# Optimization experiments

Hardware: AMD Instinct MI355X
Metric: run time of the kernel (lower is better)

The kernel has to match this reference:

```python
import jax, jax.numpy as jnp
import numpy as np
from jax import lax

B, T, C = 1, 2048, 2048
HS = 64
H = C // HS          # 32 heads
FFN = 7168
NS = 4               # packed sequences in the batch-1 stream
EPS_LN = 1e-5
EPS_GN = 1e-5 * 8 ** 2   # GroupNorm eps = 1e-5 * head_size_divisor**2


def setup_inputs() -> dict:
    key = jax.random.key(0)
    ks = iter(jax.random.split(key, 48))
    def rn(shape, s=1.0):
        return jax.random.normal(next(ks), shape, jnp.float32) * s
    sc = C ** -0.5
    return dict(
        x=rn((B, T, C)),
        start_pos=jnp.array([0, 512, 1024, 1536], dtype=jnp.int32),
        att_state=rn((NS, C)),
        wkv_state=rn((NS, H, HS, HS), 0.1),
        ffn_state=rn((NS, C)),
        ln1_g=jnp.ones((C,), jnp.float32), ln1_b=jnp.zeros((C,), jnp.float32),
        ln2_g=jnp.ones((C,), jnp.float32), ln2_b=jnp.zeros((C,), jnp.float32),
        tm_maa_x=rn((C,), 0.1), tm_maa_w=rn((C,), 0.1), tm_maa_k=rn((C,), 0.1),
        tm_maa_v=rn((C,), 0.1), tm_maa_r=rn((C,), 0.1), tm_maa_g=rn((C,), 0.1),
        tm_w1=rn((C, 160), 0.02), tm_w2=rn((5, 32, C), 0.02),
        td=rn((C,), 0.3) - 0.5, td_w1=rn((C, 64), 0.02), td_w2=rn((64, C), 0.02),
        u=rn((H, HS), 0.1),
        Wr=rn((C, C), sc), Wk=rn((C, C), sc), Wv=rn((C, C), sc),
        Wg=rn((C, C), sc), Wo=rn((C, C), sc),
        lnx_g=jnp.ones((C,), jnp.float32), lnx_b=jnp.zeros((C,), jnp.float32),
        cm_maa_k=rn((C,), 0.1), cm_maa_r=rn((C,), 0.1),
        Wck=rn((C, FFN), sc), Wcv=rn((FFN, C), FFN ** -0.5), Wcr=rn((C, C), sc),
    )


def _ln(x, g, b, eps):
    m = x.mean(-1, keepdims=True)
    v = ((x - m) ** 2).mean(-1, keepdims=True)
    return (x - m) * lax.rsqrt(v + eps) * g + b


def _shift(x, start_pos, state):
    # ZeroPad2d((0,0,1,-1)) token shift, then restore per-sequence carry state
    sh = jnp.concatenate([jnp.zeros_like(x[:, :1]), x[:, :-1]], axis=1)
    return sh.at[0, start_pos, :].set(state)


def reference(x, start_pos, att_state, wkv_state, ffn_state,
              ln1_g, ln1_b, ln2_g, ln2_b,
              tm_maa_x, tm_maa_w, tm_maa_k, tm_maa_v, tm_maa_r, tm_maa_g,
              tm_w1, tm_w2, td, td_w1, td_w2, u,
              Wr, Wk, Wv, Wg, Wo, lnx_g, lnx_b,
              cm_maa_k, cm_maa_r, Wck, Wcv, Wcr):
    is_start = jnp.zeros((T,), bool).at[start_pos].set(True)
    seq_id = jnp.clip(jnp.cumsum(is_start.astype(jnp.int32)) - 1, 0, NS - 1)

    # ---------------- Tmix (RWKV6 time mix) ----------------
    xa = _ln(x, ln1_g, ln1_b, EPS_LN)
    sh = _shift(xa, start_pos, att_state)
    xx = sh - xa
    xxx = jnp.tanh((xa + xx * tm_maa_x) @ tm_w1)                    # [B,T,160]
    mix = jnp.einsum('btse,sec->sbtc', xxx.reshape(B, T, 5, 32), tm_w2)
    mw, mk, mv, mr, mg = mix
    xw = xa + xx * (tm_maa_w + mw)
    xk = xa + xx * (tm_maa_k + mk)
    xv = xa + xx * (tm_maa_v + mv)
    xr = xa + xx * (tm_maa_r + mr)
    xg = xa + xx * (tm_maa_g + mg)
    r = (xr @ Wr).reshape(T, H, HS)
    k = (xk @ Wk).reshape(T, H, HS)
    v = (xv @ Wv).reshape(T, H, HS)
    g = jax.nn.silu(xg @ Wg)                                        # [B,T,C]
    w = td + jnp.tanh(xw @ td_w1) @ td_w2                           # [B,T,C]
    dec = jnp.exp(-jnp.exp(w)).reshape(T, H, HS)

    # continuous WKV recurrence: per-sequence state restore at starts
    def step(S, inp):
        rt, kt, vt, dt, st, sid = inp
        S = jnp.where(st, wkv_state[sid], S)                        # [H,HS,HS]
        y = jnp.einsum('hi,hij->hj', rt, S) \
            + (rt * u * kt).sum(-1, keepdims=True) * vt             # bonus term
        S = dt[:, :, None] * S + kt[:, :, None] * vt[:, None, :]
        return S, y

    _, y = lax.scan(step, jnp.zeros((H, HS, HS), jnp.float32),
                    (r, k, v, dec, is_start, seq_id))
    y = y.reshape(B, T, H, HS)
    # GroupNorm (n_head groups) fused per token/head
    mu = y.mean(-1, keepdims=True)
    var = ((y - mu) ** 2).mean(-1, keepdims=True)
    y = ((y - mu) * lax.rsqrt(var + EPS_GN)).reshape(B, T, C) * lnx_g + lnx_b
    x = x + (y * g) @ Wo

    # ---------------- CMix (channel mix) ----------------
    xf = _ln(x, ln2_g, ln2_b, EPS_LN)
    sh = _shift(xf, start_pos, ffn_state)
    xx = sh - xf
    xk = xf + xx * cm_maa_k
    xr = xf + xx * cm_maa_r
    kv = jnp.square(jax.nn.relu(xk @ Wck)) @ Wcv
    x = x + jax.nn.sigmoid(xr @ Wcr) * kv
    return x
```

## Files before the change

### kernel.cpp

```cpp
#include <hip/hip_runtime.h>
#include <stdint.h>


#define TT 2048
#define CC 2048
#define NH 32
#define HSZ 64
#define FFND 7168
#define CHUNK 32
#define NCHUNK 64

typedef __attribute__((ext_vector_type(8))) short short8;
typedef __attribute__((ext_vector_type(4))) float f32x4;

__device__ __forceinline__ float bf2f(short s){
  return __uint_as_float(((uint32_t)(uint16_t)s) << 16);
}
__device__ __forceinline__ short f2bf(float f){
  uint32_t u = __float_as_uint(f);
  u = u + 0x7fffu + ((u >> 16) & 1u);
  return (short)(u >> 16);
}

__global__ __launch_bounds__(256) void front_kernel(
    const float* __restrict__ x, const float* __restrict__ st,
    const int* __restrict__ sp, const float* __restrict__ gam,
    const float* __restrict__ bet, const float* __restrict__ maa,
    float* __restrict__ xa, float* __restrict__ xxb, short* __restrict__ z)
{
  int t = blockIdx.x, tid = threadIdx.x;
  const float* row = x + (size_t)t*CC;
  float4 a0 = *(const float4*)(row + tid*8);
  float4 a1 = *(const float4*)(row + tid*8 + 4);
  bool hp = (t > 0);
  float4 p0 = make_float4(0.f,0.f,0.f,0.f), p1 = p0;
  if(hp){
    const float* prow = x + (size_t)(t-1)*CC;
    p0 = *(const float4*)(prow + tid*8);
    p1 = *(const float4*)(prow + tid*8 + 4);
  }
  float sa  = a0.x+a0.y+a0.z+a0.w + a1.x+a1.y+a1.z+a1.w;
  float ssa = a0.x*a0.x+a0.y*a0.y+a0.z*a0.z+a0.w*a0.w
            + a1.x*a1.x+a1.y*a1.y+a1.z*a1.z+a1.w*a1.w;
  float sq  = p0.x+p0.y+p0.z+p0.w + p1.x+p1.y+p1.z+p1.w;
  float ssq = p0.x*p0.x+p0.y*p0.y+p0.z*p0.z+p0.w*p0.w
            + p1.x*p1.x+p1.y*p1.y+p1.z*p1.z+p1.w*p1.w;
  #pragma unroll
  for(int off=1; off<64; off<<=1){
    sa += __shfl_xor(sa,off); ssa += __shfl_xor(ssa,off);
    sq += __shfl_xor(sq,off); ssq += __shfl_xor(ssq,off);
  }
  __shared__ float sm[16];
  int w = tid>>6;
  if((tid&63)==0){ sm[w]=sa; sm[4+w]=ssa; sm[8+w]=sq; sm[12+w]=ssq; }
  __syncthreads();
  sa = sm[0]+sm[1]+sm[2]+sm[3];    ssa = sm[4]+sm[5]+sm[6]+sm[7];
  sq = sm[8]+sm[9]+sm[10]+sm[11];  ssq = sm[12]+sm[13]+sm[14]+sm[15];
  float mean_a = sa*(1.f/CC);
  float rstd_a = rsqrtf(ssa*(1.f/CC) - mean_a*mean_a + 1e-5f);
  float mean_q = sq*(1.f/CC);
  float rstd_q = rsqrtf(ssq*(1.f/CC) - mean_q*mean_q + 1e-5f);
  int sp0=sp[0], sp1=sp[1], sp2=sp[2], sp3=sp[3];
  bool is_start = (sp0==t)|(sp1==t)|(sp2==t)|(sp3==t);
  int sid = (sp0<=t)+(sp1<=t)+(sp2<=t)+(sp3<=t) - 1;
  sid = sid<0?0:(sid>3?3:sid);
  int c = tid*8;
  size_t base = (size_t)t*CC + c;
  float av[8] = {a0.x,a0.y,a0.z,a0.w,a1.x,a1.y,a1.z,a1.w};
  float pv[8] = {p0.x,p0.y,p0.z,p0.w,p1.x,p1.y,p1.z,p1.w};
  #pragma unroll
  for(int j=0;j<8;j++){
    float g = gam[c+j], b = bet[c+j];
    float lnt = (av[j]-mean_a)*rstd_a*g + b;
    float sh;
    if(is_start)      sh = st[(size_t)sid*CC + c + j];
    else if(hp)       sh = (pv[j]-mean_q)*rstd_q*g + b;
    else              sh = 0.f;
    float xx = sh - lnt;
    xa[base+j]  = lnt;
    xxb[base+j] = xx;
    z[base+j]   = f2bf(lnt + xx*maa[c+j]);
  }
}

__global__ __launch_bounds__(256) void ln2_fused_kernel(
    const float* __restrict__ p0, const float* __restrict__ p1,
    const float* __restrict__ xres, const float* __restrict__ gam,
    const float* __restrict__ bet, float* __restrict__ xsum,
    float* __restrict__ lnout, float eps)
{
  int t = blockIdx.x, tid = threadIdx.x;
  size_t base = (size_t)t*CC + tid*8;
  float vv[8];
  float s = 0.f, ss = 0.f;
  #pragma unroll
  for(int j=0;j<8;j++){
    float v = p0[base+j] + p1[base+j] + xres[base+j];
    vv[j] = v; s += v; ss += v*v;
    xsum[base+j] = v;
  }
  #pragma unroll
  for(int off=1; off<64; off<<=1){ s += __shfl_xor(s,off); ss += __shfl_xor(ss,off); }
  __shared__ float sm[8];
  int w = tid>>6;
  if((tid&63)==0){ sm[w]=s; sm[4+w]=ss; }
  __syncthreads();
  s = sm[0]+sm[1]+sm[2]+sm[3]; ss = sm[4]+sm[5]+sm[6]+sm[7];
  float mean = s * (1.f/CC);
  float var  = ss * (1.f/CC) - mean*mean;
  float rstd = rsqrtf(var + eps);
  int c = tid*8;
  #pragma unroll
  for(int j=0;j<8;j++) lnout[base+j] = (vv[j]-mean)*rstd*gam[c+j] + bet[c+j];
}

__global__ __launch_bounds__(256) void shift2_kernel(
    const float* __restrict__ xf, const float* __restrict__ st,
    const int* __restrict__ sp, const float* __restrict__ cmk,
    const float* __restrict__ cmr, short* __restrict__ xk2, short* __restrict__ xr2)
{
  int t = blockIdx.x, tid = threadIdx.x;
  int sp0=sp[0], sp1=sp[1], sp2=sp[2], sp3=sp[3];
  bool is_start = (sp0==t)|(sp1==t)|(sp2==t)|(sp3==t);
  int sid = (sp0<=t)+(sp1<=t)+(sp2<=t)+(sp3<=t) - 1;
  sid = sid<0?0:(sid>3?3:sid);
  int c = tid*8;
  const float* src = is_start ? (st + (size_t)sid*CC + c)
                   : (t>0 ? xf + (size_t)(t-1)*CC + c : nullptr);
  const float* cur = xf + (size_t)t*CC + c;
  size_t ix = (size_t)t*CC + c;
  #pragma unroll
  for(int jj=0;jj<8;jj++){
    float xfv = cur[jj];
    float sh = src ? src[jj] : 0.f;
    float d = sh - xfv;
    xk2[ix+jj] = f2bf(xfv + d*cmk[c+jj]);
    xr2[ix+jj] = f2bf(xfv + d*cmr[c+jj]);
  }
}

__global__ __launch_bounds__(256) void mix5_kernel(
    const float* __restrict__ xxxb, const float* __restrict__ w2,
    const float* __restrict__ xa, const float* __restrict__ xxv,
    const float* __restrict__ mw, const float* __restrict__ mk,
    const float* __restrict__ mv, const float* __restrict__ mr,
    const float* __restrict__ mg,
    short* __restrict__ ow, short* __restrict__ ok, short* __restrict__ ov,
    short* __restrict__ orr, short* __restrict__ og)
{
  int t0 = (blockIdx.x >> 3) * 8;
  int c  = ((blockIdx.x & 7) << 8) + threadIdx.x;
  float acc[5][8];
  #pragma unroll
  for(int s=0;s<5;s++)
    #pragma unroll
    for(int tt=0;tt<8;tt++) acc[s][tt]=0.f;
  #pragma unroll
  for(int s=0;s<5;s++){
    for(int e=0;e<32;e++){
      float wv = w2[(size_t)(s*32+e)*CC + c];
      #pragma unroll
      for(int tt=0;tt<8;tt++)
        acc[s][tt] += xxxb[(size_t)(t0+tt)*160 + s*32 + e] * wv;
    }
  }
  float vmw=mw[c], vmk=mk[c], vmv=mv[c], vmr=mr[c], vmg=mg[c];
  #pragma unroll
  for(int tt=0;tt<8;tt++){
    size_t ix = (size_t)(t0+tt)*CC + c;
    float av = xa[ix], xv = xxv[ix];
    ow[ix]  = f2bf(av + xv*(vmw + acc[0][tt]));
    ok[ix]  = f2bf(av + xv*(vmk + acc[1][tt]));
    ov[ix]  = f2bf(av + xv*(vmv + acc[2][tt]));
    orr[ix] = f2bf(av + xv*(vmr + acc[3][tt]));
    og[ix]  = f2bf(av + xv*(vmg + acc[4][tt]));
  }
}

__global__ __launch_bounds__(256) void dec_kernel(
    const float* __restrict__ h1b, const float* __restrict__ tw2,
    const float* __restrict__ td, float* __restrict__ out)
{
  int t0 = (blockIdx.x >> 3) * 8;
  int c  = ((blockIdx.x & 7) << 8) + threadIdx.x;
  float acc[8] = {0,0,0,0,0,0,0,0};
  for(int e=0;e<64;e++){
    float wv = tw2[(size_t)e*CC + c];
    #pragma unroll
    for(int tt=0;tt<8;tt++) acc[tt] += h1b[(size_t)(t0+tt)*64 + e]*wv;
  }
  float tdc = td[c];
  #pragma unroll
  for(int tt=0;tt<8;tt++)
    out[(size_t)(t0+tt)*CC + c] = expf(-expf(tdc + acc[tt]));
}

template<int N, int NK>
__global__ __launch_bounds__(256) void tanh_reduce_kernel(
    const float* __restrict__ part, float* __restrict__ out)
{
  int idx = blockIdx.x*256 + threadIdx.x;
  int col = idx & (N-1);
  int row = idx >> (N==256 ? 8 : 7);
  float s = 0.f;
  #pragma unroll
  for(int z=0;z<8;z++) s += part[(size_t)z*TT*N + idx];
  if(col < NK) out[(size_t)row*NK + col] = tanhf(s);
}

__global__ __launch_bounds__(256) void transpose_f2bf_kernel(
    const float* __restrict__ W, short* __restrict__ Wt, int K, int N)
{
  __shared__ float tile[64][65];
  int n0 = blockIdx.x*64, k0 = blockIdx.y*64;
  int tid = threadIdx.x;
  #pragma unroll
  for(int q=0;q<16;q++){
    int ix = q*256 + tid;
    int r = ix >> 6, cc2 = ix & 63;
    tile[r][cc2] = (n0 + cc2 < N) ? W[(size_t)(k0+r)*N + n0 + cc2] : 0.f;
  }
  __syncthreads();
  #pragma unroll
  for(int q=0;q<16;q++){
    int ix = q*256 + tid;
    int r = ix >> 6, cc2 = ix & 63;
    Wt[(size_t)(n0+r)*K + k0 + cc2] = f2bf(tile[cc2][r]);
  }
}

struct WPtr4 { const float* w[4]; };
__global__ __launch_bounds__(256) void transpose4_f2bf_kernel(
    WPtr4 ws4, short* __restrict__ Wt)
{
  __shared__ float tile[64][65];
  int z = blockIdx.z;
  const float* W = ws4.w[z];
  short* dst = Wt + (size_t)z*CC*CC;
  int n0 = blockIdx.x*64, k0 = blockIdx.y*64;
  int tid = threadIdx.x;
  #pragma unroll
  for(int q=0;q<16;q++){
    int ix = q*256 + tid;
    int r = ix >> 6, cc2 = ix & 63;
    tile[r][cc2] = W[(size_t)(k0+r)*CC + n0 + cc2];
  }
  __syncthreads();
  #pragma unroll
  for(int q=0;q<16;q++){
    int ix = q*256 + tid;
    int r = ix >> 6, cc2 = ix & 63;
    dst[(size_t)(n0+r)*CC + k0 + cc2] = f2bf(tile[cc2][r]);
  }
}

__device__ __forceinline__ void load_lds16(const void* g, void* l){
  __builtin_amdgcn_global_load_lds(
      (const __attribute__((address_space(1))) uint32_t*)g,
      (__attribute__((address_space(3))) uint32_t*)l, 16, 0, 0);
}

template<int EPI>
__global__ __launch_bounds__(256) void gemm_bt_kernel(
    const short* __restrict__ A, const short* __restrict__ Bt,
    void* __restrict__ Cout, int M, int N, int Kstride, int Klen,
    long zA, long zB, long zC)
{
  __shared__ __align__(16) short As[128*64];
  __shared__ __align__(16) short Bs[128*64];
  int z = blockIdx.z;
  const short* A0 = A + (size_t)z*zA;
  const short* B0 = Bt + (size_t)z*zB;
  int tid = threadIdx.x;
  int w = tid >> 6, lane = tid & 63;
  int l16 = lane & 15, lhi = lane >> 4;
  int wr = w >> 1, wc = w & 1;
  int gx = gridDim.x;
  int nwg = gx*gridDim.y;
  int lin = blockIdx.y*gx + blockIdx.x;
  int wg = (lin & 7)*(nwg >> 3) + (lin >> 3);
  int bn = wg % gx, bm = wg / gx;
  const short* Ab = A0 + (size_t)bm*128*Kstride;
  const short* Bb = B0 + (size_t)bn*128*Kstride;
  int srow = w*8 + (lane>>3);
  int scol = lane & 7;
  f32x4 acc[4][4] = {};
  for(int kt=0; kt<Klen; kt+=64){
    __syncthreads();
    #pragma unroll
    for(int q=0;q<4;q++){
      int row = q*32 + srow;
      int c8 = scol ^ (row & 7);
      int ldsoff = (q*256 + w*64)*8;
      load_lds16(Ab + (size_t)row*Kstride + kt + c8*8, As + ldsoff);
      load_lds16(Bb + (size_t)row*Kstride + kt + c8*8, Bs + ldsoff);
    }
    __syncthreads();
    #pragma unroll
    for(int kk=0;kk<2;kk++){
      short8 af[4], bf[4];
      #pragma unroll
      for(int m=0;m<4;m++){
        int row = wr*64 + m*16 + l16;
        int slot = (kk*4 + lhi) ^ (row & 7);
        af[m] = *(const short8*)(As + row*64 + slot*8);
      }
      #pragma unroll
      for(int n=0;n<4;n++){
        int row = wc*64 + n*16 + l16;
        int slot = (kk*4 + lhi) ^ (row & 7);
        bf[n] = *(const short8*)(Bs + row*64 + slot*8);
      }
      #pragma unroll
      for(int m=0;m<4;m++){
        #pragma unroll
        for(int n=0;n<4;n++)
          acc[m][n] = __builtin_amdgcn_mfma_f32_16x16x32_bf16(af[m], bf[n], acc[m][n], 0, 0, 0);
      }
    }
  }
  int m0 = bm*128 + wr*64;
  int n0 = bn*128 + wc*64;
  #pragma unroll
  for(int m=0;m<4;m++){
    #pragma unroll
    for(int n=0;n<4;n++){
      #pragma unroll
      for(int jj=0;jj<4;jj++){
        int row = m0 + m*16 + lhi*4 + jj;
        int col = n0 + n*16 + l16;
        size_t ix = (size_t)row*N + col;
        float val = acc[m][n][jj];
        if constexpr (EPI==0){ ((short*)Cout)[(size_t)z*zC + ix] = f2bf(val); }
        else if constexpr (EPI==3){ float rv = fmaxf(val, 0.f); ((short*)Cout)[ix] = f2bf(rv*rv); }
        else if constexpr (EPI==5){ ((float*)Cout)[(size_t)z*zC + ix] = val; }
        else {
          short* o = (short*)Cout + (size_t)z*zC;
          o[ix] = (z==3) ? f2bf(val/(1.f+expf(-val))) : f2bf(val);
        }
      }
    }
  }
}

template<int EPI>
__global__ __launch_bounds__(512, 1) void gemm256_kernel(
    const short* __restrict__ A, const short* __restrict__ Bt,
    void* __restrict__ Cout, int M, int N, int Kstride, int Klen,
    long zA, long zB, long zC)
{
  __shared__ __align__(16) short As[2][256*64];
  __shared__ __align__(16) short Bs[2][256*64];
  int z = blockIdx.z;
  const short* A0p = A + (size_t)z*zA;
  const short* B0p = Bt + (size_t)z*zB;
  int tid = threadIdx.x;
  int w = tid >> 6, lane = tid & 63;
  int l16 = lane & 15, lhi = lane >> 4;
  int wr = w >> 2, wc = w & 3;
  int gx = gridDim.x;
  int nwg = gx*gridDim.y;
  int lin = blockIdx.y*gx + blockIdx.x;
  int wg = (lin & 7)*(nwg >> 3) + (lin >> 3);
  int bn = wg % gx, bm = wg / gx;
  const short* Ab = A0p + (size_t)bm*256*Kstride;
  const short* Bb = B0p + (size_t)bn*256*Kstride;
  int srow_w = w*8 + (lane>>3);
  int scol = lane & 7;
  f32x4 acc[8][4] = {};

  auto STG = [&](const short* src, short* dst, int half, int kt){
    #pragma unroll
    for(int q=0;q<2;q++){
      int row = half*128 + q*64 + srow_w;
      int c8 = scol ^ (row & 7);
      load_lds16(src + (size_t)row*Kstride + kt + c8*8,
                 dst + (half*128 + q*64 + w*8)*64);
    }
  };
  auto DSA = [&](const short* Ac, int p, short8 afr[2][2]){
    #pragma unroll
    for(int mm=0;mm<2;mm++)
      #pragma unroll
      for(int kk=0;kk<2;kk++){
        int row = wr*128 + (p*2+mm)*16 + l16;
        int slot = (kk*4 + lhi) ^ (row & 7);
        afr[mm][kk] = *(const short8*)(Ac + row*64 + slot*8);
      }
  };
  auto DSB = [&](const short* Bc, short8 bfr[4][2]){
    #pragma unroll
    for(int n=0;n<4;n++)
      #pragma unroll
      for(int kk=0;kk<2;kk++){
        int row = wc*64 + n*16 + l16;
        int slot = (kk*4 + lhi) ^ (row & 7);
        bfr[n][kk] = *(const short8*)(Bc + row*64 + slot*8);
      }
  };
  auto MM = [&](int p, short8 afr[2][2], short8 bfr[4][2]){
    __builtin_amdgcn_s_setprio(1);
    #pragma unroll
    for(int mm=0;mm<2;mm++)
      #pragma unroll
      for(int n=0;n<4;n++)
        #pragma unroll
        for(int kk=0;kk<2;kk++)
          acc[p*2+mm][n] = __builtin_amdgcn_mfma_f32_16x16x32_bf16(
              afr[mm][kk], bfr[n][kk], acc[p*2+mm][n], 0, 0, 0);
    __builtin_amdgcn_s_setprio(0);
  };
  #define LG0()  do{ asm volatile("s_waitcnt lgkmcnt(0)" ::: "memory"); \
      __builtin_amdgcn_sched_barrier(0); }while(0)
  #define BARX() do{ __builtin_amdgcn_s_barrier(); \
      __builtin_amdgcn_sched_barrier(0); }while(0)

  int NT = Klen >> 6;
  int niter = NT >> 1;
  STG(Ab, &As[0][0], 0, 0); STG(Ab, &As[0][0], 1, 0);
  STG(Bb, &Bs[0][0], 0, 0); STG(Bb, &Bs[0][0], 1, 0);
  STG(Bb, &Bs[1][0], 0, 64); STG(Bb, &Bs[1][0], 1, 64);
  asm volatile("s_waitcnt vmcnt(4)" ::: "memory");
  BARX();

  for(int i=0;i<niter;++i){
    int kt_o  = (2*i+1) << 6;
    int kt_e2 = (2*i+2) << 6;
    int kt_o2 = (2*i+3) << 6;
    bool st = (i+1 < niter);
    short8 bfr[4][2], afr[2][2];
    DSB(&Bs[0][0], bfr);
    DSA(&As[0][0], 0, afr);
    STG(Ab, &As[1][0], 0, kt_o);
    LG0(); MM(0, afr, bfr);
    DSA(&As[0][0], 1, afr);
    STG(Ab, &As[1][0], 1, kt_o);
    LG0(); MM(1, afr, bfr);
    BARX();
    DSA(&As[0][0], 2, afr);
    if(st) STG(Bb, &Bs[0][0], 0, kt_e2);
    LG0(); MM(2, afr, bfr);
    DSA(&As[0][0], 3, afr);
    if(st){ STG(Bb, &Bs[0][0], 1, kt_e2);
            asm volatile("s_waitcnt vmcnt(4)" ::: "memory"); }
    else  { asm volatile("s_waitcnt vmcnt(0)" ::: "memory"); }
    LG0(); MM(3, afr, bfr);
    BARX();
    DSB(&Bs[1][0], bfr);
    DSA(&As[1][0], 0, afr);
    if(st) STG(Ab, &As[0][0], 0, kt_e2);
    LG0(); MM(0, afr, bfr);
    DSA(&As[1][0], 1, afr);
    if(st) STG(Ab, &As[0][0], 1, kt_e2);
    LG0(); MM(1, afr, bfr);
    BARX();
    DSA(&As[1][0], 2, afr);
    if(st) STG(Bb, &Bs[1][0], 0, kt_o2);
    LG0(); MM(2, afr, bfr);
    DSA(&As[1][0], 3, afr);
    if(st){ STG(Bb, &Bs[1][0], 1, kt_o2);
            asm volatile("s_waitcnt vmcnt(4)" ::: "memory"); }
    else  { asm volatile("s_waitcnt vmcnt(0)" ::: "memory"); }
    LG0(); MM(3, afr, bfr);
    BARX();
  }
  #undef LG0
  #undef BARX

  int m0 = bm*256 + wr*128;
  int n0 = bn*256 + wc*64;
  #pragma unroll
  for(int m=0;m<8;m++){
    #pragma unroll
    for(int n=0;n<4;n++){
      #pragma unroll
      for(int jj=0;jj<4;jj++){
        int row = m0 + m*16 + lhi*4 + jj;
        int col = n0 + n*16 + l16;
        size_t ix = (size_t)row*N + col;
        float val = acc[m][n][jj];
        if constexpr (EPI==3){ float rv = fmaxf(val, 0.f); ((short*)Cout)[ix] = f2bf(rv*rv); }
        else if constexpr (EPI==5){ ((float*)Cout)[(size_t)z*zC + ix] = val; }
        else {
          short* o = (short*)Cout + (size_t)z*zC;
          o[ix] = (z==3) ? f2bf(val/(1.f+expf(-val))) : f2bf(val);
        }
      }
    }
  }
}

__global__ __launch_bounds__(256) void wkv_chunk_kernel(
    const short* __restrict__ rb, const short* __restrict__ kb,
    const short* __restrict__ vb, const float* __restrict__ db,
    const float* __restrict__ wkv_state, const float* __restrict__ u,
    const int* __restrict__ sp,
    float* __restrict__ yb, short* __restrict__ rtb,
    float* __restrict__ Bc, float* __restrict__ Pc)
{
  int blk = blockIdx.x;
  int ch = blk >> 5;
  int h  = blk & 31;
  int tid = threadIdx.x;
  int a = tid & 3, j = tid >> 2;
  int w = tid >> 6, lane = tid & 63;
  __shared__ float sr[2][64], sk[2][64], suk[2][64], sv[2][64], sd[2][64];
  __shared__ float sp_[64];
  float u_reg = (w==1) ? u[h*64 + lane] : 0.f;
  if(tid < 64) sp_[tid] = 1.f;
  float S[16];
  #pragma unroll
  for(int ii=0;ii<16;ii++) S[ii]=0.f;
  int sp0=sp[0], sp1=sp[1], sp2=sp[2], sp3=sp[3];
  int tbase = ch*CHUNK;
  {
    size_t gb = (size_t)tbase*CC + h*64;
    if(w==0)      sr[0][lane] = bf2f(rb[gb+lane]);
    else if(w==1){ float kv_=bf2f(kb[gb+lane]); sk[0][lane]=kv_; suk[0][lane]=u_reg*kv_; }
    else if(w==2) sv[0][lane] = bf2f(vb[gb+lane]);
    else          sd[0][lane] = db[gb+lane];
  }
  __syncthreads();
  for(int tl=0; tl<CHUNK; ++tl){
    int t = tbase + tl;
    int buf = tl & 1;
    if(tl+1 < CHUNK){
      size_t nb = (size_t)(t+1)*CC + h*64;
      int b2_ = buf^1;
      if(w==0)      sr[b2_][lane] = bf2f(rb[nb+lane]);
      else if(w==1){ float kv_=bf2f(kb[nb+lane]); sk[b2_][lane]=kv_; suk[b2_][lane]=u_reg*kv_; }
      else if(w==2) sv[b2_][lane] = bf2f(vb[nb+lane]);
      else          sd[b2_][lane] = db[nb+lane];
    }
    size_t base = (size_t)t*CC + h*64;
    bool is_start = (sp0==t)|(sp1==t)|(sp2==t)|(sp3==t);
    if(is_start){
      int sid = (sp0<=t)+(sp1<=t)+(sp2<=t)+(sp3<=t) - 1;
      sid = sid<0?0:(sid>3?3:sid);
      const float* wsrc = wkv_state + (((size_t)sid*NH + h)*HSZ + a*16)*HSZ + j;
      #pragma unroll
      for(int ii=0;ii<16;ii++) S[ii] = wsrc[(size_t)ii*HSZ];
      if(tid < 64) sp_[tid] = 0.f;
    }
    float vj = sv[buf][j];
    float yp = 0.f, bp = 0.f;
    #pragma unroll
    for(int ii=0;ii<16;ii++){
      int i = a*16 + ii;
      float ri = sr[buf][i];
      yp += ri * S[ii];
      bp += ri * suk[buf][i];
    }
    yp += __shfl_xor(yp, 1); yp += __shfl_xor(yp, 2);
    bp += __shfl_xor(bp, 1); bp += __shfl_xor(bp, 2);
    if(a == 0) yb[base + j] = yp + bp*vj;
    if(tid < 64){
      rtb[base + tid] = f2bf(sr[buf][tid] * sp_[tid]);
      sp_[tid] *= sd[buf][tid];
    }
    #pragma unroll
    for(int ii=0;ii<16;ii++){
      int i = a*16 + ii;
      S[ii] = sd[buf][i]*S[ii] + sk[buf][i]*vj;
    }
    __syncthreads();
  }
  size_t cb = ((size_t)ch*NH + h)*HSZ*HSZ;
  #pragma unroll
  for(int ii=0;ii<16;ii++) Bc[cb + (size_t)(a*16+ii)*HSZ + j] = S[ii];
  if(tid < 64) Pc[((size_t)ch*NH + h)*HSZ + tid] = sp_[tid];
}

__global__ __launch_bounds__(256) void wkv_combine_kernel(
    float* __restrict__ BS, const float* __restrict__ Pc)
{
  int idx = blockIdx.x*256 + threadIdx.x;
  int hi = idx >> 6;
  float s = 0.f;
  for(int cc=0; cc<NCHUNK; ++cc){
    size_t ix = (size_t)cc*(NH*HSZ*HSZ) + idx;
    float b = BS[ix];
    BS[ix] = s;
    s = Pc[cc*(NH*HSZ) + hi]*s + b;
  }
}

__global__ __launch_bounds__(256) void wkv_corr_gn_kernel(
    const short* __restrict__ rtb, const float* __restrict__ Sin,
    const float* __restrict__ yb, const short* __restrict__ gb,
    const float* __restrict__ gam, const float* __restrict__ bet,
    short* __restrict__ yg)
{
  int blk = blockIdx.x;
  int ch = blk >> 5, h = blk & 31;
  __shared__ float Ssm[64][64];
  __shared__ float Rsm[32][65];
  int tid = threadIdx.x;
  const float* Sp = Sin + (size_t)(ch*NH + h)*HSZ*HSZ;
  #pragma unroll
  for(int q=0;q<16;q++) ((float*)Ssm)[q*256+tid] = Sp[q*256+tid];
  #pragma unroll
  for(int q=0;q<8;q++){
    int ix = q*256 + tid;
    int tl = ix>>6, i = ix&63;
    Rsm[tl][i] = bf2f(rtb[(size_t)(ch*CHUNK+tl)*CC + h*64 + i]);
  }
  __syncthreads();
  int tl = tid >> 3;
  int jq = tid & 7;
  float acc[8];
  #pragma unroll
  for(int jj=0;jj<8;jj++) acc[jj]=0.f;
  for(int i=0;i<64;i++){
    float rv = Rsm[tl][i];
    #pragma unroll
    for(int jj=0;jj<8;jj++) acc[jj] += rv * Ssm[i][jq*8+jj];
  }
  int t = ch*CHUNK + tl;
  float val[8];
  float s = 0.f, ss = 0.f;
  #pragma unroll
  for(int jj=0;jj<8;jj++){
    float v = yb[(size_t)t*CC + h*64 + jq*8+jj] + acc[jj];
    val[jj] = v; s += v; ss += v*v;
  }
  #pragma unroll
  for(int off=1; off<8; off<<=1){ s += __shfl_xor(s,off); ss += __shfl_xor(ss,off); }
  float mu = s*(1.f/64.f);
  float var = ss*(1.f/64.f) - mu*mu;
  float rstd = rsqrtf(var + 6.4e-4f);
  #pragma unroll
  for(int jj=0;jj<8;jj++){
    int cc = h*64 + jq*8+jj;
    float o = (val[jj]-mu)*rstd*gam[cc] + bet[cc];
    yg[(size_t)t*CC + cc] = f2bf(o * bf2f(gb[(size_t)t*CC + cc]));
  }
}

__global__ __launch_bounds__(256) void final_kernel(
    const float* __restrict__ s0, const float* __restrict__ s1,
    const float* __restrict__ kv0, const float* __restrict__ kv1,
    const float* __restrict__ kv2, const float* __restrict__ kv3,
    float* __restrict__ out)
{
  size_t i = ((size_t)blockIdx.x*256 + threadIdx.x)*8;
  #pragma unroll
  for(int j=0;j<8;j++){
    float sv = s0[i+j] + s1[i+j];
    float sig = 1.f/(1.f + expf(-sv));
    out[i+j] = out[i+j] + sig*(kv0[i+j] + kv1[i+j] + kv2[i+j] + kv3[i+j]);
  }
}

extern "C" void kernel_launch(void* const* d_in, const int* in_sizes, int n_in,
                              void* d_out, int out_size, void* d_ws, size_t ws_size,
                              hipStream_t stream)
{
  (void)in_sizes; (void)n_in; (void)out_size;
  const float* x         = (const float*)d_in[0];
  const int*   sp        = (const int*)d_in[1];
  const float* att_state = (const float*)d_in[2];
  const float* wkv_state = (const float*)d_in[3];
  const float* ffn_state = (const float*)d_in[4];
  const float* ln1_g=(const float*)d_in[5],  *ln1_b=(const float*)d_in[6];
  const float* ln2_g=(const float*)d_in[7],  *ln2_b=(const float*)d_in[8];
  const float* maa_x=(const float*)d_in[9],  *maa_w=(const float*)d_in[10], *maa_k=(const float*)d_in[11];
  const float* maa_v=(const float*)d_in[12], *maa_r=(const float*)d_in[13], *maa_g=(const float*)d_in[14];
  const float* tm_w1=(const float*)d_in[15], *tm_w2=(const float*)d_in[16];
  const float* td=(const float*)d_in[17],    *td_w1=(const float*)d_in[18], *td_w2=(const float*)d_in[19];
  const float* u = (const float*)d_in[20];
  const float* Wr=(const float*)d_in[21], *Wk=(const float*)d_in[22], *Wv=(const float*)d_in[23];
  const float* Wg=(const float*)d_in[24], *Wo=(const float*)d_in[25];
  const float* lnx_g=(const float*)d_in[26], *lnx_b=(const float*)d_in[27];
  const float* cm_k=(const float*)d_in[28],  *cm_r=(const float*)d_in[29];
  const float* Wck=(const float*)d_in[30], *Wcv=(const float*)d_in[31], *Wcr=(const float*)d_in[32];

  char* ws = (char*)d_ws;
  const size_t SLOT  = (size_t)TT*CC*4;
  const size_t BSLOT = (size_t)TT*CC*2;
  const size_t WT_SZ = (size_t)4*CC*CC*2;
  const size_t NEED  = 6*SLOT + 10*BSLOT + WT_SZ + (4u<<20);
  if(ws_size < NEED) return;

  float* xa   = (float*)(ws + 0*SLOT);
  float* xxb  = (float*)(ws + 1*SLOT);
  float* zw   = (float*)(ws + 2*SLOT);
  float* decb = (float*)(ws + 3*SLOT);
  float* yb   = (float*)(ws + 4*SLOT);
  float* S5   = (float*)(ws + 5*SLOT);
  float* BS   = xa;
  float* xxxPart = zw;
  float* h1Part  = yb;
  short* bA   = (short*)(ws + 6*SLOT);
  short* bO   = (short*)(ws + 6*SLOT + 4*BSLOT);
  short* b1 = bO + 0*(TT*CC);
  short* b2 = bO + 1*(TT*CC);
  short* b3 = bO + 2*(TT*CC);
  short* b4 = bO + 3*(TT*CC);
  short* b5 = bO + 4*(TT*CC);
  short* b6 = bO + 5*(TT*CC);
  short* WT = (short*)(ws + 6*SLOT + 10*BSLOT);
  char*  aux = (char*)WT + WT_SZ;
  float* xxxb = (float*)(aux);
  float* h1b  = (float*)(aux + (2u<<20));
  float* Pc   = (float*)(aux + (5u<<19));
  float* xmid = (float*)d_out;

  dim3 B256(256), B512(512);
  const int NTC8 = TT*CC/8/256;

  front_kernel<<<TT, B256, 0, stream>>>(x, att_state, sp, ln1_g, ln1_b, maa_x,
                                        xa, xxb, bA);
  transpose_f2bf_kernel<<<dim3(4, CC/64), B256, 0, stream>>>(tm_w1, WT, CC, 160);
  gemm_bt_kernel<5><<<dim3(2, TT/128, 8), B256, 0, stream>>>(bA, WT, xxxPart, TT, 256, CC, 256,
      256, 256, (long)TT*256);
  tanh_reduce_kernel<256,160><<<TT, B256, 0, stream>>>(xxxPart, xxxb);
  mix5_kernel<<<NTC8, B256, 0, stream>>>(xxxb, tm_w2, xa, xxb,
      maa_w, maa_k, maa_v, maa_r, maa_g,
      b5, bA + 1*(TT*CC), bA + 2*(TT*CC), bA, bA + 3*(TT*CC));
  transpose_f2bf_kernel<<<dim3(2, CC/64), B256, 0, stream>>>(td_w1, WT, CC, 64);
  gemm_bt_kernel<5><<<dim3(1, TT/128, 8), B256, 0, stream>>>(b5, WT, h1Part, TT, 128, CC, 256,
      256, 256, (long)TT*128);
  tanh_reduce_kernel<128,64><<<TT/2, B256, 0, stream>>>(h1Part, h1b);
  dec_kernel<<<NTC8, B256, 0, stream>>>(h1b, td_w2, td, decb);

  WPtr4 w4; w4.w[0]=Wr; w4.w[1]=Wk; w4.w[2]=Wv; w4.w[3]=Wg;
  transpose4_f2bf_kernel<<<dim3(CC/64, CC/64, 4), B256, 0, stream>>>(w4, WT);
  gemm256_kernel<6><<<dim3(CC/256, TT/256, 4), B512, 0, stream>>>(bA, WT, b1, TT, CC, CC, CC,
      (long)TT*CC, (long)CC*CC, (long)TT*CC);

  wkv_chunk_kernel<<<NCHUNK*NH, B256, 0, stream>>>(b1, b2, b3, decb, wkv_state, u, sp,
                                                   yb, b5, BS, Pc);
  wkv_combine_kernel<<<NH*HSZ*HSZ/256, B256, 0, stream>>>(BS, Pc);
  wkv_corr_gn_kernel<<<NCHUNK*NH, B256, 0, stream>>>(b5, BS, yb, b4, lnx_g, lnx_b, b6);

  transpose_f2bf_kernel<<<dim3(CC/64, CC/64), B256, 0, stream>>>(Wo, WT, CC, CC);
  gemm_bt_kernel<5><<<dim3(CC/128, TT/128, 2), B256, 0, stream>>>(b6, WT, yb, TT, CC, CC, 1024,
      1024, 1024, (long)TT*CC);
  ln2_fused_kernel<<<TT, B256, 0, stream>>>(yb, S5, x, ln2_g, ln2_b, xmid, zw, 1e-5f);

  shift2_kernel<<<TT, B256, 0, stream>>>(zw, ffn_state, sp, cm_k, cm_r, bA, bA + 1*(TT*CC));
  transpose_f2bf_kernel<<<dim3(FFND/64, CC/64), B256, 0, stream>>>(Wck, WT, CC, FFND);
  gemm256_kernel<3><<<dim3(FFND/256, TT/256, 1), B512, 0, stream>>>(bA, WT, b1, TT, FFND, CC, CC,
      0, 0, 0);
  transpose_f2bf_kernel<<<dim3(CC/64, FFND/64), B256, 0, stream>>>(Wcv, WT, FFND, CC);
  gemm256_kernel<5><<<dim3(CC/256, TT/256, 4), B512, 0, stream>>>(b1, WT, zw, TT, CC, FFND, 1792,
      1792, 1792, (long)TT*CC);
  transpose_f2bf_kernel<<<dim3(CC/64, CC/64), B256, 0, stream>>>(Wcr, WT, CC, CC);
  gemm_bt_kernel<5><<<dim3(CC/128, TT/128, 2), B256, 0, stream>>>(bA + 1*(TT*CC), WT, xa, TT, CC, CC, 1024,
      1024, 1024, (long)TT*CC);
  final_kernel<<<NTC8, B256, 0, stream>>>(xa, xxb, zw, decb, yb, S5, xmid);
}
```

Measured before the change: 689.9 us.

## Make WKV chunk kernel wave-private to remove per-step block barriers

```diff
diff --git a/kernel.cpp b/kernel.cpp
--- a/kernel.cpp
+++ b/kernel.cpp
@@ -499,38 +499,38 @@
     float* __restrict__ Bc, float* __restrict__ Pc)
 {
   int blk = blockIdx.x;
-  int ch = blk >> 5;
-  int h  = blk & 31;
+  int ch = blk >> 5, h = blk & 31;
   int tid = threadIdx.x;
-  int a = tid & 3, j = tid >> 2;
   int w = tid >> 6, lane = tid & 63;
-  __shared__ float sr[2][64], sk[2][64], suk[2][64], sv[2][64], sd[2][64];
-  __shared__ float sp_[64];
-  float u_reg = (w==1) ? u[h*64 + lane] : 0.f;
-  if(tid < 64) sp_[tid] = 1.f;
+  int a = lane >> 4, jloc = lane & 15;
+  int j = w*16 + jloc;
+  __shared__ __align__(16) float sr[4][2][64], sd[4][2][64], sk[4][2][64];
+  float u_reg = u[h*64 + lane];
   float S[16];
   #pragma unroll
   for(int ii=0;ii<16;ii++) S[ii]=0.f;
+  float p_reg = 1.f;
   int sp0=sp[0], sp1=sp[1], sp2=sp[2], sp3=sp[3];
   int tbase = ch*CHUNK;
-  {
-    size_t gb = (size_t)tbase*CC + h*64;
-    if(w==0)      sr[0][lane] = bf2f(rb[gb+lane]);
-    else if(w==1){ float kv_=bf2f(kb[gb+lane]); sk[0][lane]=kv_; suk[0][lane]=u_reg*kv_; }
-    else if(w==2) sv[0][lane] = bf2f(vb[gb+lane]);
-    else          sd[0][lane] = db[gb+lane];
-  }
-  __syncthreads();
+  size_t gb0 = (size_t)tbase*CC + h*64 + lane;
+  float r_c = bf2f(rb[gb0]);
+  float k_c0 = bf2f(kb[gb0]);
+  float v_c = bf2f(vb[gb0]);
+  float d_c = db[gb0];
+  sr[w][0][lane] = r_c; sd[w][0][lane] = d_c; sk[w][0][lane] = k_c0;
+  float m0s = r_c * u_reg * k_c0;
+  #pragma unroll
+  for(int off=1; off<64; off<<=1) m0s += __shfl_xor(m0s, off);
+  float bsum_c = m0s;
+
   for(int tl=0; tl<CHUNK; ++tl){
     int t = tbase + tl;
     int buf = tl & 1;
-    if(tl+1 < CHUNK){
-      size_t nb = (size_t)(t+1)*CC + h*64;
-      int b2_ = buf^1;
-      if(w==0)      sr[b2_][lane] = bf2f(rb[nb+lane]);
-      else if(w==1){ float kv_=bf2f(kb[nb+lane]); sk[b2_][lane]=kv_; suk[b2_][lane]=u_reg*kv_; }
-      else if(w==2) sv[b2_][lane] = bf2f(vb[nb+lane]);
-      else          sd[b2_][lane] = db[nb+lane];
+    bool more = (tl+1 < CHUNK);
+    short r_n=0, k_n=0, v_n=0; float d_n=0.f;
+    if(more){
+      size_t nb = (size_t)(t+1)*CC + h*64 + lane;
+      r_n = rb[nb]; k_n = kb[nb]; v_n = vb[nb]; d_n = db[nb];
     }
     size_t base = (size_t)t*CC + h*64;
     bool is_start = (sp0==t)|(sp1==t)|(sp2==t)|(sp3==t);
@@ -540,35 +540,44 @@
       const float* wsrc = wkv_state + (((size_t)sid*NH + h)*HSZ + a*16)*HSZ + j;
       #pragma unroll
       for(int ii=0;ii<16;ii++) S[ii] = wsrc[(size_t)ii*HSZ];
-      if(tid < 64) sp_[tid] = 0.f;
-    }
-    float vj = sv[buf][j];
-    float yp = 0.f, bp = 0.f;
-    #pragma unroll
-    for(int ii=0;ii<16;ii++){
-      int i = a*16 + ii;
-      float ri = sr[buf][i];
-      yp += ri * S[ii];
-      bp += ri * suk[buf][i];
-    }
-    yp += __shfl_xor(yp, 1); yp += __shfl_xor(yp, 2);
-    bp += __shfl_xor(bp, 1); bp += __shfl_xor(bp, 2);
-    if(a == 0) yb[base + j] = yp + bp*vj;
-    if(tid < 64){
-      rtb[base + tid] = f2bf(sr[buf][tid] * sp_[tid]);
-      sp_[tid] *= sd[buf][tid];
-    }
-    #pragma unroll
-    for(int ii=0;ii<16;ii++){
-      int i = a*16 + ii;
-      S[ii] = sd[buf][i]*S[ii] + sk[buf][i]*vj;
-    }
-    __syncthreads();
+      p_reg = 0.f;
+    }
+    float vj = __shfl(v_c, j);
+    const float4* rp = (const float4*)&sr[w][buf][a*16];
+    const float4* dp = (const float4*)&sd[w][buf][a*16];
+    const float4* kp = (const float4*)&sk[w][buf][a*16];
+    float yp = 0.f;
+    #pragma unroll
+    for(int q=0;q<4;q++){
+      float4 R = rp[q], D = dp[q], K = kp[q];
+      yp += R.x*S[q*4+0] + R.y*S[q*4+1] + R.z*S[q*4+2] + R.w*S[q*4+3];
+      S[q*4+0] = D.x*S[q*4+0] + K.x*vj;
+      S[q*4+1] = D.y*S[q*4+1] + K.y*vj;
+      S[q*4+2] = D.z*S[q*4+2] + K.z*vj;
+      S[q*4+3] = D.w*S[q*4+3] + K.w*vj;
+    }
+    yp += __shfl_xor(yp, 16);
+    yp += __shfl_xor(yp, 32);
+    if(a == 0) yb[base + j] = yp + bsum_c * vj;
+    if(w == 0){
+      rtb[base + lane] = f2bf(r_c * p_reg);
+      p_reg *= d_c;
+    }
+    if(more){
+      float rf = bf2f(r_n), kf = bf2f(k_n), vf = bf2f(v_n);
+      int nb2 = buf^1;
+      sr[w][nb2][lane] = rf; sd[w][nb2][lane] = d_n; sk[w][nb2][lane] = kf;
+      float mm = rf * u_reg * kf;
+      #pragma unroll
+      for(int off=1; off<64; off<<=1) mm += __shfl_xor(mm, off);
+      bsum_c = mm;
+      r_c = rf; d_c = d_n; v_c = vf;
+    }
   }
   size_t cb = ((size_t)ch*NH + h)*HSZ*HSZ;
   #pragma unroll
   for(int ii=0;ii<16;ii++) Bc[cb + (size_t)(a*16+ii)*HSZ + j] = S[ii];
-  if(tid < 64) Pc[((size_t)ch*NH + h)*HSZ + tid] = sp_[tid];
+  if(w == 0) Pc[((size_t)ch*NH + h)*HSZ + lane] = p_reg;
 }
 
 __global__ __launch_bounds__(256) void wkv_combine_kernel(
```

After: 686.7 us. No clear change (-0.5%).
